# Kernel tuning notes

Hardware: AMD Instinct MI355X
Metric: run time of the kernel (lower is better)

## Reference

```python
import jax, jax.numpy as jnp
import numpy as np

N_NODES = 50000
N_EDGES = 800000
D = 128          # d_model
N_LAYER = 4
N_GRAPHS = 128
N_IDS = 256      # nn.Embedding(256, d_model)


def setup_inputs() -> dict:
    key = jax.random.key(0)
    ks = jax.random.split(key, 10)
    s = 0.02
    return {
        "position_feature": jax.random.normal(ks[0], (N_NODES, 3), dtype=jnp.float32),
        "id_feature": jax.random.randint(ks[1], (N_NODES,), 0, N_IDS),
        "edge_index": jax.random.randint(ks[2], (2, N_EDGES), 0, N_NODES),
        "batch": jnp.sort(jax.random.randint(ks[3], (N_NODES,), 0, N_GRAPHS)),
        "num_graphs": N_GRAPHS,
        "Wp": jax.random.normal(ks[4], (3, D), dtype=jnp.float32) * s,
        "bp": jnp.zeros((D,), jnp.float32),
        "id_emb": jax.random.normal(ks[5], (N_IDS, D), dtype=jnp.float32) * s,
        "Wn": jax.random.normal(ks[6], (2 * D, D), dtype=jnp.float32) * s,
        "bn": jnp.zeros((D,), jnp.float32),
        "conv_W": jax.random.normal(ks[7], (N_LAYER, D, D), dtype=jnp.float32) * s,
        "conv_b": jnp.zeros((N_LAYER, D), jnp.float32),
        "Wa": jax.random.normal(ks[8], ((1 + N_LAYER) * D, D), dtype=jnp.float32) * s,
        "ba": jnp.zeros((D,), jnp.float32),
    }


def _gcn(x, W, b, src, dst, norm, n):
    # PyG GCNConv: h = x @ W; out[dst] += norm(e) * h[src]; out += bias
    h = x @ W
    msg = h[src] * norm[:, None]
    return jax.ops.segment_sum(msg, dst, num_segments=n) + b


def reference(position_feature, id_feature, edge_index, batch, num_graphs,
              Wp, bp, id_emb, Wn, bn, conv_W, conv_b, Wa, ba):
    n = position_feature.shape[0]
    # GCN normalization with self-loops (shared across all layers)
    loops = jnp.arange(n)
    src = jnp.concatenate([edge_index[0], loops])
    dst = jnp.concatenate([edge_index[1], loops])
    deg = jax.ops.segment_sum(jnp.ones_like(src, dtype=position_feature.dtype), dst, num_segments=n)
    dinv = jnp.where(deg > 0, jax.lax.rsqrt(deg), 0.0)
    norm = dinv[src] * dinv[dst]  # [E + N]

    pos = jax.nn.relu(position_feature @ Wp + bp)       # [N, D]
    idf = jax.nn.relu(id_emb[id_feature])               # [N, D]
    x = jax.nn.relu(jnp.concatenate([pos, idf], axis=1) @ Wn + bn)  # [N, D]

    gs = [jax.ops.segment_max(x, batch, num_segments=num_graphs)]   # g_embed_0
    h = x
    for l in range(conv_W.shape[0]):
        h = jax.nn.relu(_gcn(h, conv_W[l], conv_b[l], src, dst, norm, n))
        gs.append(jax.ops.segment_max(h, batch, num_segments=num_graphs))

    g_embed = jnp.concatenate(gs, axis=1)  # [G, (1+n_layer)*D]
    return g_embed @ Wa + ba               # [G, D]
```

## Files before the change

### kernel.cpp

```cpp
#include <hip/hip_runtime.h>

#define N_NODES 50000
#define N_EDGES 800000
#define D 128
#define NLAYER 4
#define NGRAPH 128
#define GDIM (5 * D)
#define NBUCK 196
#define BCAP 4608

typedef __attribute__((ext_vector_type(8))) short bf16x8;
typedef __attribute__((ext_vector_type(4))) float f32x4;

__device__ __forceinline__ float b2f(unsigned short u) {
    return __uint_as_float(((unsigned)u) << 16);
}
__device__ __forceinline__ unsigned short f2b(float f) {
    unsigned u = __float_as_uint(f);
    unsigned r = (u + 0x7fffu + ((u >> 16) & 1u)) >> 16;
    return (unsigned short)r;
}


__global__ __launch_bounds__(256) void k_bucket(
    const int* __restrict__ esrc, const int* __restrict__ edst,
    int* __restrict__ bcnt_rel, int* __restrict__ ebuf) {
    __shared__ int hcnt[NBUCK];
    __shared__ int hbase[NBUCK];
    int t = threadIdx.x;
    for (int i = t; i < NBUCK; i += 256) hcnt[i] = 0;
    __syncthreads();
    int e0 = blockIdx.x * 1024 + t;
    int d[4], s[4];
#pragma unroll
    for (int i = 0; i < 4; ++i) {
        int e = e0 + i * 256;
        if (e < N_EDGES) {
            d[i] = edst[e];
            s[i] = esrc[e];
            atomicAdd(&hcnt[d[i] >> 8], 1);
        } else {
            d[i] = -1;
        }
    }
    __syncthreads();
    for (int i = t; i < NBUCK; i += 256) {
        int c = hcnt[i];
        hbase[i] = (c > 0) ? (i * BCAP + atomicAdd(&bcnt_rel[i], c)) : 0;
        hcnt[i] = 0;
    }
    __syncthreads();
#pragma unroll
    for (int i = 0; i < 4; ++i) {
        if (d[i] >= 0) {
            int b = d[i] >> 8;
            int p = atomicAdd(&hcnt[b], 1);
            int pos = hbase[b] + p;
            if (pos < (b + 1) * BCAP)
                ebuf[pos] = (s[i] & 0xffff) | ((d[i] & 255) << 16);
        }
    }
}


__global__ void k_bscan(const int* __restrict__ bcnt_rel, int* __restrict__ bbase) {
    __shared__ int lds[256];
    int t = threadIdx.x;
    int v = (t < NBUCK) ? bcnt_rel[t] : 0;
    lds[t] = v;
    __syncthreads();
    int tot = v;
    for (int off = 1; off < 256; off <<= 1) {
        int add = (t >= off) ? lds[t - off] : 0;
        __syncthreads();
        tot += add;
        lds[t] = tot;
        __syncthreads();
    }
    if (t < NBUCK) bbase[t] = tot - v;
}


__global__ __launch_bounds__(256) void k_fillB1(
    const int* __restrict__ ebuf, const int* __restrict__ bcnt_rel,
    const int* __restrict__ bbase, const int* __restrict__ batch,
    int* __restrict__ offs, int* __restrict__ cnt, float* __restrict__ dinv,
    int* __restrict__ hist2) {
    __shared__ int lcnt[256];
    __shared__ int lscan[256];
    int b = blockIdx.x, t = threadIdx.x;
    lcnt[t] = 0;
    __syncthreads();
    int s0 = b * BCAP, s1 = b * BCAP + bcnt_rel[b];
    for (int i = s0 + t; i < s1; i += 256)
        atomicAdd(&lcnt[(ebuf[i] >> 16) & 255], 1);
    __syncthreads();
    int v = lcnt[t];
    lscan[t] = v;
    __syncthreads();
    int tot = v;
    for (int off = 1; off < 256; off <<= 1) {
        int add = (t >= off) ? lscan[t - off] : 0;
        __syncthreads();
        tot += add;
        lscan[t] = tot;
        __syncthreads();
    }
    int node = (b << 8) + t;
    if (node < N_NODES) {
        offs[node] = bbase[b] + (tot - v);
        cnt[node] = v;
        dinv[node] = 1.f / sqrtf((float)(v + 1));
        atomicAdd(&hist2[batch[node] * 128 + min(v, 127)], 1);
    }
}


__global__ __launch_bounds__(256) void k_fillB2(
    const int* __restrict__ ebuf, const int* __restrict__ bcnt_rel,
    const int* __restrict__ offs, const float* __restrict__ dinv,
    unsigned int* __restrict__ csrs) {
    __shared__ int loffs[256];
    __shared__ int lcnt[256];
    __shared__ float ldinv[256];
    int b = blockIdx.x, t = threadIdx.x;
    int nbase = b << 8;
    if (nbase + t < N_NODES) {
        loffs[t] = offs[nbase + t];
        ldinv[t] = dinv[nbase + t];
    }
    lcnt[t] = 0;
    __syncthreads();
    int s0 = b * BCAP, s1 = b * BCAP + bcnt_rel[b];
    for (int i = s0 + t; i < s1; i += 256) {
        int pk = ebuf[i];
        int ld = (pk >> 16) & 255;
        int src = pk & 0xffff;
        float w = dinv[src] * ldinv[ld];
        int p = atomicAdd(&lcnt[ld], 1);
        csrs[loffs[ld] + p] = (unsigned)src | ((unsigned)f2b(w) << 16);
    }
}

__global__ __launch_bounds__(1024) void k_scan16k(int* __restrict__ hist2) {
    __shared__ int lds[1024];
    int t = threadIdx.x;
    int v[16];
    int s = 0;
#pragma unroll
    for (int j = 0; j < 16; ++j) { v[j] = hist2[t * 16 + j]; s += v[j]; }
    lds[t] = s;
    __syncthreads();
    int tot = s;
    for (int off = 1; off < 1024; off <<= 1) {
        int add = (t >= off) ? lds[t - off] : 0;
        __syncthreads();
        tot += add;
        lds[t] = tot;
        __syncthreads();
    }
    int run = tot - s;
#pragma unroll
    for (int j = 0; j < 16; ++j) { hist2[t * 16 + j] = run; run += v[j]; }
}

__global__ void k_scatter(const int* __restrict__ cnt, const int* __restrict__ batch,
                          int* __restrict__ hist2, int* __restrict__ perm) {
    int i = blockIdx.x * 256 + threadIdx.x;
    if (i < N_NODES) {
        int key = batch[i] * 128 + min(cnt[i], 127);
        int p = atomicAdd(&hist2[key], 1);
        perm[p] = i;
    }
}


__global__ __launch_bounds__(256) void k_prep(
    const float* __restrict__ Wn, const float* __restrict__ convW,
    unsigned short* __restrict__ Wpack,
    const float* __restrict__ id_emb, float* __restrict__ T) {
    int blk = blockIdx.x;
    if (blk < 320) {
        int tid = blk * 256 + threadIdx.x;
        int m = tid >> 14;
        int rem = tid & 16383;
        int ct = rem >> 11, kc = (rem >> 9) & 3, l = (rem >> 3) & 63, j = rem & 7;
        int k = kc * 32 + ((l >> 4) * 8) + j;
        int n = ct * 16 + (l & 15);
        const float* src = (m == 0) ? Wn : (convW + (size_t)(m - 1) * 16384);
        Wpack[tid] = f2b(src[k * 128 + n]);
    } else {
        int t = threadIdx.x;
        int d = t & 127;
        int r = (blk - 320) * 2 + (t >> 7);
        float acc = 0.f;
        for (int k = 0; k < 128; ++k)
            acc = fmaf(fmaxf(id_emb[r * 128 + k], 0.f), Wn[(128 + k) * 128 + d], acc);
        T[r * 128 + d] = acc;
    }
}


__global__ __launch_bounds__(256) void k_encoder(
    const float* __restrict__ pos, const int* __restrict__ idfeat,
    const float* __restrict__ Wp, const float* __restrict__ bp,
    const unsigned short* __restrict__ WpackE, const float* __restrict__ bn,
    const float* __restrict__ T, unsigned short* __restrict__ A16,
    const int* __restrict__ batch, float* __restrict__ gbuf) {
    __shared__ unsigned short feat[64 * 128];
    __shared__ float posl[192];
    __shared__ int bbat[64];
    int t = threadIdx.x;
    int base = blockIdx.x * 64;
    int avail = N_NODES - base;
    if (t < 192) {
        int idx = base * 3 + t;
        posl[t] = (idx < N_NODES * 3) ? pos[idx] : 0.f;
    }
    if (t < 64) bbat[t] = (base + t < N_NODES) ? batch[base + t] : -1;
    __syncthreads();
#pragma unroll
    for (int i = 0; i < 4; ++i) {
        int gid = t + i * 256;
        int row = gid >> 4, kg = gid & 15;
        unsigned short u[8];
        if (row < avail) {
            float p0 = posl[row * 3], p1 = posl[row * 3 + 1], p2 = posl[row * 3 + 2];
#pragma unroll
            for (int j = 0; j < 8; ++j) {
                int d = kg * 8 + j;
                float v = fmaf(p0, Wp[d], fmaf(p1, Wp[128 + d], fmaf(p2, Wp[256 + d], bp[d])));
                u[j] = f2b(fmaxf(v, 0.f));
            }
        } else {
#pragma unroll
            for (int j = 0; j < 8; ++j) u[j] = 0;
        }
        char* dst = (char*)feat + row * 256 + ((kg * 16) ^ ((row & 7) << 4));
        *(uint4*)dst = *(uint4*)u;
    }
    __syncthreads();
    int wid = t >> 6, l = t & 63;
    int r0 = wid * 16;
    f32x4 acc[8];
#pragma unroll
    for (int ct = 0; ct < 8; ++ct) acc[ct] = (f32x4){0.f, 0.f, 0.f, 0.f};
    const bf16x8* wp = (const bf16x8*)WpackE;
#pragma unroll
    for (int kc = 0; kc < 4; ++kc) {
        int row = r0 + (l & 15);
        const char* ap = (const char*)feat + row * 256 +
                         ((kc * 64 + ((l >> 4) * 16)) ^ ((row & 7) << 4));
        bf16x8 afrag = *(const bf16x8*)ap;
#pragma unroll
        for (int ct = 0; ct < 8; ++ct) {
            bf16x8 bfrag = wp[(ct * 4 + kc) * 64 + l];
            acc[ct] = __builtin_amdgcn_mfma_f32_16x16x32_bf16(afrag, bfrag, acc[ct], 0, 0, 0);
        }
    }
    int subrow = (l >> 4) * 4, col0 = l & 15;
    int ids[4];
#pragma unroll
    for (int i = 0; i < 4; ++i) {
        int node = base + r0 + subrow + i;
        ids[i] = (node < N_NODES) ? idfeat[node] : 0;
    }
    __syncthreads();
#pragma unroll
    for (int ct = 0; ct < 8; ++ct) {
        int col = ct * 16 + col0;
        float bcol = bn[col];
#pragma unroll
        for (int i = 0; i < 4; ++i) {
            int node = base + r0 + subrow + i;
            unsigned short ob = 0;
            if (node < N_NODES) {
                float v = acc[ct][i] + bcol + T[ids[i] * 128 + col];
                ob = f2b(fmaxf(v, 0.f));
                A16[(size_t)node * 128 + col] = ob;
            }
            feat[(r0 + subrow + i) * 128 + col] = ob;
        }
    }
    __syncthreads();
    if (t < 128) {
        int j = 0;
        while (j < 64) {
            int g = bbat[j];
            float m = b2f(feat[j * 128 + t]);
            int k = j + 1;
            while (k < 64 && bbat[k] == g) { m = fmaxf(m, b2f(feat[k * 128 + t])); ++k; }
            if (g >= 0) atomicMax((int*)&gbuf[g * GDIM + t], __float_as_int(m));
            j = k;
        }
    }
}


__global__ __launch_bounds__(256) void k_layer(
    const unsigned short* __restrict__ Hin, unsigned short* __restrict__ Hout,
    const unsigned short* __restrict__ WpackL,
    const int* __restrict__ offs, const int* __restrict__ cnt,
    const unsigned int* __restrict__ csrs, const float* __restrict__ dinv,
    const float* __restrict__ bias, const int* __restrict__ batch,
    const int* __restrict__ perm, float* __restrict__ gbuf, int goff) {
    __shared__ unsigned short hagg[16 * 128];
    __shared__ float smx[16][132];
    __shared__ int bb[16];
    __shared__ int snode[16];
    int tid = threadIdx.x;
    int wave = tid >> 6, lane = tid & 63;
    int q = lane >> 4, l16 = lane & 15;
    int row = wave * 4 + q;
    int nbase = blockIdx.x * 16;
    if (tid < 16) {
        int n = perm[nbase + tid];
        snode[tid] = n;
        bb[tid] = batch[n];
    }
    int node = perm[nbase + row];

    int start = offs[node];
    int c = cnt[node];
    float di = dinv[node];
    float sw = di * di;
    const uint4* B4 = (const uint4*)Hin;
    float a[8];
    {
        uint4 sv = B4[(size_t)node * 16 + l16];
        a[0] = sw * __uint_as_float(sv.x << 16);
        a[1] = sw * __uint_as_float(sv.x & 0xffff0000u);
        a[2] = sw * __uint_as_float(sv.y << 16);
        a[3] = sw * __uint_as_float(sv.y & 0xffff0000u);
        a[4] = sw * __uint_as_float(sv.z << 16);
        a[5] = sw * __uint_as_float(sv.z & 0xffff0000u);
        a[6] = sw * __uint_as_float(sv.w << 16);
        a[7] = sw * __uint_as_float(sv.w & 0xffff0000u);
    }
    int j = 0;
    for (; j + 8 <= c; j += 8) {
        unsigned pk[8];
        uint4 v[8];
#pragma unroll
        for (int i = 0; i < 8; ++i) pk[i] = csrs[start + j + i];
#pragma unroll
        for (int i = 0; i < 8; ++i) v[i] = B4[(size_t)(pk[i] & 0xffffu) * 16 + l16];
#pragma unroll
        for (int i = 0; i < 8; ++i) {
            float w = __uint_as_float(pk[i] & 0xffff0000u);
            a[0] = fmaf(w, __uint_as_float(v[i].x << 16), a[0]);
            a[1] = fmaf(w, __uint_as_float(v[i].x & 0xffff0000u), a[1]);
            a[2] = fmaf(w, __uint_as_float(v[i].y << 16), a[2]);
            a[3] = fmaf(w, __uint_as_float(v[i].y & 0xffff0000u), a[3]);
            a[4] = fmaf(w, __uint_as_float(v[i].z << 16), a[4]);
            a[5] = fmaf(w, __uint_as_float(v[i].z & 0xffff0000u), a[5]);
            a[6] = fmaf(w, __uint_as_float(v[i].w << 16), a[6]);
            a[7] = fmaf(w, __uint_as_float(v[i].w & 0xffff0000u), a[7]);
        }
    }
    for (; j < c; ++j) {
        unsigned pk = csrs[start + j];
        float w = __uint_as_float(pk & 0xffff0000u);
        uint4 v = B4[(size_t)(pk & 0xffffu) * 16 + l16];
        a[0] = fmaf(w, __uint_as_float(v.x << 16), a[0]);
        a[1] = fmaf(w, __uint_as_float(v.x & 0xffff0000u), a[1]);
        a[2] = fmaf(w, __uint_as_float(v.y << 16), a[2]);
        a[3] = fmaf(w, __uint_as_float(v.y & 0xffff0000u), a[3]);
        a[4] = fmaf(w, __uint_as_float(v.z << 16), a[4]);
        a[5] = fmaf(w, __uint_as_float(v.z & 0xffff0000u), a[5]);
        a[6] = fmaf(w, __uint_as_float(v.w << 16), a[6]);
        a[7] = fmaf(w, __uint_as_float(v.w & 0xffff0000u), a[7]);
    }
    {
        unsigned u[4];
#pragma unroll
        for (int k = 0; k < 4; ++k)
            u[k] = (unsigned)f2b(a[2 * k]) | ((unsigned)f2b(a[2 * k + 1]) << 16);
        char* dst = (char*)hagg + row * 256 + ((l16 * 16) ^ ((row & 7) << 4));
        *(uint4*)dst = *(uint4*)u;
    }
    __syncthreads();

    f32x4 oacc[2] = {(f32x4){0.f, 0.f, 0.f, 0.f}, (f32x4){0.f, 0.f, 0.f, 0.f}};
    const bf16x8* wp = (const bf16x8*)WpackL;
#pragma unroll
    for (int kc = 0; kc < 4; ++kc) {
        int arow = lane & 15;
        const char* ap = (const char*)hagg + arow * 256 +
                         ((kc * 64 + ((lane >> 4) * 16)) ^ ((arow & 7) << 4));
        bf16x8 afrag = *(const bf16x8*)ap;
#pragma unroll
        for (int ci = 0; ci < 2; ++ci) {
            int ct = wave * 2 + ci;
            bf16x8 bfrag = wp[(ct * 4 + kc) * 64 + lane];
            oacc[ci] = __builtin_amdgcn_mfma_f32_16x16x32_bf16(afrag, bfrag, oacc[ci], 0, 0, 0);
        }
    }

    int subrow = (lane >> 4) * 4;
#pragma unroll
    for (int ci = 0; ci < 2; ++ci) {
        int col = (wave * 2 + ci) * 16 + (lane & 15);
        float bcol = bias[col];
#pragma unroll
        for (int i = 0; i < 4; ++i) {
            int r = subrow + i;
            float v = fmaxf(oacc[ci][i] + bcol, 0.f);
            smx[r][col] = v;
            Hout[(size_t)snode[r] * 128 + col] = f2b(v);
        }
    }
    __syncthreads();
    if (tid < 128) {
        int jj = 0;
        while (jj < 16) {
            int g = bb[jj];
            float m = smx[jj][tid];
            int k = jj + 1;
            while (k < 16 && bb[k] == g) { m = fmaxf(m, smx[k][tid]); ++k; }
            atomicMax((int*)&gbuf[g * GDIM + goff + tid], __float_as_int(m));
            jj = k;
        }
    }
}


__global__ __launch_bounds__(128) void k_final(const float* __restrict__ gbuf,
                                               const float* __restrict__ Wa,
                                               const float* __restrict__ ba,
                                               float* __restrict__ out) {
    __shared__ float gr[GDIM];
    int g = blockIdx.x, t = threadIdx.x;
    for (int i = t; i < GDIM; i += 128) gr[i] = gbuf[g * GDIM + i];
    __syncthreads();
    float acc = ba[t];
    for (int k = 0; k < GDIM; ++k) acc = fmaf(gr[k], Wa[k * 128 + t], acc);
    out[g * 128 + t] = acc;
}


extern "C" void kernel_launch(void* const* d_in, const int* in_sizes, int n_in,
                              void* d_out, int out_size, void* d_ws, size_t ws_size,
                              hipStream_t stream) {
    const float* pos    = (const float*)d_in[0];
    const int*   idfeat = (const int*)d_in[1];
    const int*   eidx   = (const int*)d_in[2];
    const int*   batch  = (const int*)d_in[3];
    const float* Wp     = (const float*)d_in[5];
    const float* bp     = (const float*)d_in[6];
    const float* id_emb = (const float*)d_in[7];
    const float* Wn     = (const float*)d_in[8];
    const float* bn     = (const float*)d_in[9];
    const float* convW  = (const float*)d_in[10];
    const float* convb  = (const float*)d_in[11];
    const float* Wa     = (const float*)d_in[12];
    const float* ba     = (const float*)d_in[13];
    float* out = (float*)d_out;

    const int* esrc = eidx;
    const int* edst = eidx + N_EDGES;

    char* w = (char*)d_ws;
    auto alloc = [&](size_t bytes) -> char* {
        char* p = w;
        w += (bytes + 255) & ~(size_t)255;
        return p;
    };
    char* zstart = w;
    float* gbuf     = (float*)alloc((size_t)NGRAPH * GDIM * 4);
    int*   hist2    = (int*)alloc((size_t)16384 * 4);
    int*   bcnt_rel = (int*)alloc((size_t)NBUCK * 4);
    size_t zbytes = (size_t)(w - zstart);

    int*   cnt  = (int*)alloc((size_t)N_NODES * 4);
    unsigned short* A16a = (unsigned short*)alloc((size_t)N_NODES * D * 2);
    unsigned short* A16b = (unsigned short*)alloc((size_t)N_NODES * D * 2);
    float* dinv = (float*)alloc((size_t)N_NODES * 4);
    int*   offs = (int*)alloc((size_t)(N_NODES + 1) * 4);
    int*   bbase= (int*)alloc((NBUCK + 1) * 4);
    unsigned int* csrs = (unsigned int*)alloc((size_t)N_EDGES * 4);
    int*   ebuf = (int*)alloc((size_t)NBUCK * BCAP * 4);
    int*   perm = (int*)alloc((size_t)N_NODES * 4);
    float* T    = (float*)alloc((size_t)256 * D * 4);
    unsigned short* Wpack = (unsigned short*)alloc((size_t)5 * 16384 * 2);

    hipMemsetAsync(zstart, 0, zbytes, stream);

    k_bucket<<<(N_EDGES + 1023) / 1024, 256, 0, stream>>>(esrc, edst, bcnt_rel, ebuf);
    k_bscan<<<1, 256, 0, stream>>>(bcnt_rel, bbase);
    k_fillB1<<<NBUCK, 256, 0, stream>>>(ebuf, bcnt_rel, bbase, batch, offs, cnt, dinv, hist2);
    k_scan16k<<<1, 1024, 0, stream>>>(hist2);
    k_scatter<<<(N_NODES + 255) / 256, 256, 0, stream>>>(cnt, batch, hist2, perm);
    k_fillB2<<<NBUCK, 256, 0, stream>>>(ebuf, bcnt_rel, offs, dinv, csrs);

    k_prep<<<448, 256, 0, stream>>>(Wn, convW, Wpack, id_emb, T);
    k_encoder<<<(N_NODES + 63) / 64, 256, 0, stream>>>(pos, idfeat, Wp, bp, Wpack, bn, T,
                                                       A16a, batch, gbuf);

    unsigned short* Hin = A16a;
    unsigned short* Hout = A16b;
    for (int l = 0; l < NLAYER; ++l) {
        k_layer<<<N_NODES / 16, 256, 0, stream>>>(Hin, Hout, Wpack + (size_t)(l + 1) * 16384,
                                                  offs, cnt, csrs, dinv,
                                                  convb + (size_t)l * D, batch, perm, gbuf,
                                                  (l + 1) * D);
        unsigned short* tmp = Hin; Hin = Hout; Hout = tmp;
    }

    k_final<<<NGRAPH, 128, 0, stream>>>(gbuf, Wa, ba, out);
}
```

Before: 260.7 us.

## Process 32 nodes per block in GCN layer with dual interleaved gathers

Each k_layer block now handles 32 nodes instead of 16. Each 16-lane group gathers neighbours for two nodes at once, interleaving their loads 4 at a time to expose more memory-level parallelism. Each B-fragment load of the weights now feeds two MFMA row tiles, and the per-block max buffer is stored as bf16 to save LDS. The hipMemsetAsync is replaced with a custom zeroing kernel. The trade-off is fewer blocks, more registers per thread, and load imbalance when the two nodes have very different degrees.

```diff
diff --git a/kernel.cpp b/kernel.cpp
--- a/kernel.cpp
+++ b/kernel.cpp
@@ -19,6 +19,23 @@
     unsigned u = __float_as_uint(f);
     unsigned r = (u + 0x7fffu + ((u >> 16) & 1u)) >> 16;
     return (unsigned short)r;
+}
+__device__ __forceinline__ void fma8(float* a, unsigned pkw, uint4 v) {
+    float w = __uint_as_float(pkw & 0xffff0000u);
+    a[0] = fmaf(w, __uint_as_float(v.x << 16), a[0]);
+    a[1] = fmaf(w, __uint_as_float(v.x & 0xffff0000u), a[1]);
+    a[2] = fmaf(w, __uint_as_float(v.y << 16), a[2]);
+    a[3] = fmaf(w, __uint_as_float(v.y & 0xffff0000u), a[3]);
+    a[4] = fmaf(w, __uint_as_float(v.z << 16), a[4]);
+    a[5] = fmaf(w, __uint_as_float(v.z & 0xffff0000u), a[5]);
+    a[6] = fmaf(w, __uint_as_float(v.w << 16), a[6]);
+    a[7] = fmaf(w, __uint_as_float(v.w & 0xffff0000u), a[7]);
+}
+
+
+__global__ void k_zero(uint4* __restrict__ p, int n16) {
+    int i = blockIdx.x * 256 + threadIdx.x;
+    if (i < n16) p[i] = make_uint4(0u, 0u, 0u, 0u);
 }
 
 
@@ -304,96 +321,155 @@
     const unsigned int* __restrict__ csrs, const float* __restrict__ dinv,
     const float* __restrict__ bias, const int* __restrict__ batch,
     const int* __restrict__ perm, float* __restrict__ gbuf, int goff) {
-    __shared__ unsigned short hagg[16 * 128];
-    __shared__ float smx[16][132];
-    __shared__ int bb[16];
-    __shared__ int snode[16];
+    __shared__ unsigned short hagg[32 * 128];
+    __shared__ unsigned short smx[32 * 136];
+    __shared__ int bb[32];
+    __shared__ int snode[32];
     int tid = threadIdx.x;
     int wave = tid >> 6, lane = tid & 63;
-    int q = lane >> 4, l16 = lane & 15;
-    int row = wave * 4 + q;
-    int nbase = blockIdx.x * 16;
-    if (tid < 16) {
-        int n = perm[nbase + tid];
-        snode[tid] = n;
-        bb[tid] = batch[n];
-    }
-    int node = perm[nbase + row];
-
-    int start = offs[node];
-    int c = cnt[node];
-    float di = dinv[node];
-    float sw = di * di;
+    int r = tid >> 4;
+    int l16 = tid & 15;
+    int nbase = blockIdx.x * 32;
+    if (tid < 32) {
+        int idx = nbase + tid;
+        if (idx < N_NODES) {
+            int n = perm[idx];
+            snode[tid] = n;
+            bb[tid] = batch[n];
+        } else {
+            snode[tid] = 0;
+            bb[tid] = -1;
+        }
+    }
+    int idx0 = nbase + r;
+    int idx1 = nbase + 16 + r;
+    int node0 = perm[idx0];
+    bool val1 = idx1 < N_NODES;
+    int node1 = val1 ? perm[idx1] : 0;
+
     const uint4* B4 = (const uint4*)Hin;
-    float a[8];
+    int start0 = offs[node0], c0 = cnt[node0];
+    float di0 = dinv[node0];
+    int start1 = val1 ? offs[node1] : 0;
+    int c1 = val1 ? cnt[node1] : 0;
+    float di1 = val1 ? dinv[node1] : 0.f;
+
+    float a0[8], a1[8];
     {
-        uint4 sv = B4[(size_t)node * 16 + l16];
-        a[0] = sw * __uint_as_float(sv.x << 16);
-        a[1] = sw * __uint_as_float(sv.x & 0xffff0000u);
-        a[2] = sw * __uint_as_float(sv.y << 16);
-        a[3] = sw * __uint_as_float(sv.y & 0xffff0000u);
-        a[4] = sw * __uint_as_float(sv.z << 16);
-        a[5] = sw * __uint_as_float(sv.z & 0xffff0000u);
-        a[6] = sw * __uint_as_float(sv.w << 16);
-        a[7] = sw * __uint_as_float(sv.w & 0xffff0000u);
-    }
-    int j = 0;
-    for (; j + 8 <= c; j += 8) {
-        unsigned pk[8];
-        uint4 v[8];
-#pragma unroll
-        for (int i = 0; i < 8; ++i) pk[i] = csrs[start + j + i];
-#pragma unroll
-        for (int i = 0; i < 8; ++i) v[i] = B4[(size_t)(pk[i] & 0xffffu) * 16 + l16];
-#pragma unroll
-        for (int i = 0; i < 8; ++i) {
-            float w = __uint_as_float(pk[i] & 0xffff0000u);
-            a[0] = fmaf(w, __uint_as_float(v[i].x << 16), a[0]);
-            a[1] = fmaf(w, __uint_as_float(v[i].x & 0xffff0000u), a[1]);
-            a[2] = fmaf(w, __uint_as_float(v[i].y << 16), a[2]);
-            a[3] = fmaf(w, __uint_as_float(v[i].y & 0xffff0000u), a[3]);
-            a[4] = fmaf(w, __uint_as_float(v[i].z << 16), a[4]);
-            a[5] = fmaf(w, __uint_as_float(v[i].z & 0xffff0000u), a[5]);
-            a[6] = fmaf(w, __uint_as_float(v[i].w << 16), a[6]);
-            a[7] = fmaf(w, __uint_as_float(v[i].w & 0xffff0000u), a[7]);
-        }
-    }
-    for (; j < c; ++j) {
-        unsigned pk = csrs[start + j];
-        float w = __uint_as_float(pk & 0xffff0000u);
-        uint4 v = B4[(size_t)(pk & 0xffffu) * 16 + l16];
-        a[0] = fmaf(w, __uint_as_float(v.x << 16), a[0]);
-        a[1] = fmaf(w, __uint_as_float(v.x & 0xffff0000u), a[1]);
-        a[2] = fmaf(w, __uint_as_float(v.y << 16), a[2]);
-        a[3] = fmaf(w, __uint_as_float(v.y & 0xffff0000u), a[3]);
-        a[4] = fmaf(w, __uint_as_float(v.z << 16), a[4]);
-        a[5] = fmaf(w, __uint_as_float(v.z & 0xffff0000u), a[5]);
-        a[6] = fmaf(w, __uint_as_float(v.w << 16), a[6]);
-        a[7] = fmaf(w, __uint_as_float(v.w & 0xffff0000u), a[7]);
+        uint4 sv = B4[(size_t)node0 * 16 + l16];
+        float sw = di0 * di0;
+        a0[0] = sw * __uint_as_float(sv.x << 16);
+        a0[1] = sw * __uint_as_float(sv.x & 0xffff0000u);
+        a0[2] = sw * __uint_as_float(sv.y << 16);
+        a0[3] = sw * __uint_as_float(sv.y & 0xffff0000u);
+        a0[4] = sw * __uint_as_float(sv.z << 16);
+        a0[5] = sw * __uint_as_float(sv.z & 0xffff0000u);
+        a0[6] = sw * __uint_as_float(sv.w << 16);
+        a0[7] = sw * __uint_as_float(sv.w & 0xffff0000u);
+    }
+    if (val1) {
+        uint4 sv = B4[(size_t)node1 * 16 + l16];
+        float sw = di1 * di1;
+        a1[0] = sw * __uint_as_float(sv.x << 16);
+        a1[1] = sw * __uint_as_float(sv.x & 0xffff0000u);
+        a1[2] = sw * __uint_as_float(sv.y << 16);
+        a1[3] = sw * __uint_as_float(sv.y & 0xffff0000u);
+        a1[4] = sw * __uint_as_float(sv.z << 16);
+        a1[5] = sw * __uint_as_float(sv.z & 0xffff0000u);
+        a1[6] = sw * __uint_as_float(sv.w << 16);
+        a1[7] = sw * __uint_as_float(sv.w & 0xffff0000u);
+    } else {
+#pragma unroll
+        for (int i = 0; i < 8; ++i) a1[i] = 0.f;
+    }
+
+    int j0 = 0, j1 = 0;
+    while (j0 + 4 <= c0 && j1 + 4 <= c1) {
+        unsigned p0[4], p1[4];
+        uint4 v0[4], v1[4];
+#pragma unroll
+        for (int i = 0; i < 4; ++i) p0[i] = csrs[start0 + j0 + i];
+#pragma unroll
+        for (int i = 0; i < 4; ++i) p1[i] = csrs[start1 + j1 + i];
+#pragma unroll
+        for (int i = 0; i < 4; ++i) v0[i] = B4[(size_t)(p0[i] & 0xffffu) * 16 + l16];
+#pragma unroll
+        for (int i = 0; i < 4; ++i) v1[i] = B4[(size_t)(p1[i] & 0xffffu) * 16 + l16];
+#pragma unroll
+        for (int i = 0; i < 4; ++i) fma8(a0, p0[i], v0[i]);
+#pragma unroll
+        for (int i = 0; i < 4; ++i) fma8(a1, p1[i], v1[i]);
+        j0 += 4;
+        j1 += 4;
+    }
+    for (; j0 + 4 <= c0; j0 += 4) {
+        unsigned p0[4];
+        uint4 v0[4];
+#pragma unroll
+        for (int i = 0; i < 4; ++i) p0[i] = csrs[start0 + j0 + i];
+#pragma unroll
+        for (int i = 0; i < 4; ++i) v0[i] = B4[(size_t)(p0[i] & 0xffffu) * 16 + l16];
+#pragma unroll
+        for (int i = 0; i < 4; ++i) fma8(a0, p0[i], v0[i]);
+    }
+    for (; j0 < c0; ++j0) {
+        unsigned pk = csrs[start0 + j0];
+        fma8(a0, pk, B4[(size_t)(pk & 0xffffu) * 16 + l16]);
+    }
+    for (; j1 + 4 <= c1; j1 += 4) {
+        unsigned p1[4];
+        uint4 v1[4];
+#pragma unroll
+        for (int i = 0; i < 4; ++i) p1[i] = csrs[start1 + j1 + i];
+#pragma unroll
+        for (int i = 0; i < 4; ++i) v1[i] = B4[(size_t)(p1[i] & 0xffffu) * 16 + l16];
+#pragma unroll
+        for (int i = 0; i < 4; ++i) fma8(a1, p1[i], v1[i]);
+    }
+    for (; j1 < c1; ++j1) {
+        unsigned pk = csrs[start1 + j1];
+        fma8(a1, pk, B4[(size_t)(pk & 0xffffu) * 16 + l16]);
     }
     {
         unsigned u[4];
 #pragma unroll
         for (int k = 0; k < 4; ++k)
-            u[k] = (unsigned)f2b(a[2 * k]) | ((unsigned)f2b(a[2 * k + 1]) << 16);
-        char* dst = (char*)hagg + row * 256 + ((l16 * 16) ^ ((row & 7) << 4));
+            u[k] = (unsigned)f2b(a0[2 * k]) | ((unsigned)f2b(a0[2 * k + 1]) << 16);
+        char* dst = (char*)hagg + r * 256 + ((l16 * 16) ^ ((r & 7) << 4));
         *(uint4*)dst = *(uint4*)u;
-    }
-    __syncthreads();
-
-    f32x4 oacc[2] = {(f32x4){0.f, 0.f, 0.f, 0.f}, (f32x4){0.f, 0.f, 0.f, 0.f}};
+        int r1 = r + 16;
+#pragma unroll
+        for (int k = 0; k < 4; ++k)
+            u[k] = (unsigned)f2b(a1[2 * k]) | ((unsigned)f2b(a1[2 * k + 1]) << 16);
+        dst = (char*)hagg + r1 * 256 + ((l16 * 16) ^ ((r1 & 7) << 4));
+        *(uint4*)dst = *(uint4*)u;
+    }
+    __syncthreads();
+
+    f32x4 oacc[2][2];
+#pragma unroll
+    for (int rt = 0; rt < 2; ++rt)
+#pragma unroll
+        for (int ci = 0; ci < 2; ++ci) oacc[rt][ci] = (f32x4){0.f, 0.f, 0.f, 0.f};
     const bf16x8* wp = (const bf16x8*)WpackL;
 #pragma unroll
     for (int kc = 0; kc < 4; ++kc) {
-        int arow = lane & 15;
-        const char* ap = (const char*)hagg + arow * 256 +
-                         ((kc * 64 + ((lane >> 4) * 16)) ^ ((arow & 7) << 4));
-        bf16x8 afrag = *(const bf16x8*)ap;
+        bf16x8 afrag[2];
+#pragma unroll
+        for (int rt = 0; rt < 2; ++rt) {
+            int arow = rt * 16 + (lane & 15);
+            const char* ap = (const char*)hagg + arow * 256 +
+                             ((kc * 64 + ((lane >> 4) * 16)) ^ ((arow & 7) << 4));
+            afrag[rt] = *(const bf16x8*)ap;
+        }
 #pragma unroll
         for (int ci = 0; ci < 2; ++ci) {
             int ct = wave * 2 + ci;
             bf16x8 bfrag = wp[(ct * 4 + kc) * 64 + lane];
-            oacc[ci] = __builtin_amdgcn_mfma_f32_16x16x32_bf16(afrag, bfrag, oacc[ci], 0, 0, 0);
+#pragma unroll
+            for (int rt = 0; rt < 2; ++rt)
+                oacc[rt][ci] = __builtin_amdgcn_mfma_f32_16x16x32_bf16(afrag[rt], bfrag,
+                                                                      oacc[rt][ci], 0, 0, 0);
         }
     }
 
@@ -403,22 +479,29 @@
         int col = (wave * 2 + ci) * 16 + (lane & 15);
         float bcol = bias[col];
 #pragma unroll
-        for (int i = 0; i < 4; ++i) {
-            int r = subrow + i;
-            float v = fmaxf(oacc[ci][i] + bcol, 0.f);
-            smx[r][col] = v;
-            Hout[(size_t)snode[r] * 128 + col] = f2b(v);
+        for (int rt = 0; rt < 2; ++rt) {
+#pragma unroll
+            for (int i = 0; i < 4; ++i) {
+                int row = rt * 16 + subrow + i;
+                float v = fmaxf(oacc[rt][ci][i] + bcol, 0.f);
+                unsigned short ob = f2b(v);
+                if (bb[row] >= 0)
+                    Hout[(size_t)snode[row] * 128 + col] = ob;
+                else
+                    ob = 0;
+                smx[row * 136 + col] = ob;
+            }
         }
     }
     __syncthreads();
     if (tid < 128) {
         int jj = 0;
-        while (jj < 16) {
+        while (jj < 32) {
             int g = bb[jj];
-            float m = smx[jj][tid];
+            float m = b2f(smx[jj * 136 + tid]);
             int k = jj + 1;
-            while (k < 16 && bb[k] == g) { m = fmaxf(m, smx[k][tid]); ++k; }
-            atomicMax((int*)&gbuf[g * GDIM + goff + tid], __float_as_int(m));
+            while (k < 32 && bb[k] == g) { m = fmaxf(m, b2f(smx[k * 136 + tid])); ++k; }
+            if (g >= 0) atomicMax((int*)&gbuf[g * GDIM + goff + tid], __float_as_int(m));
             jj = k;
         }
     }
@@ -484,7 +567,8 @@
     float* T    = (float*)alloc((size_t)256 * D * 4);
     unsigned short* Wpack = (unsigned short*)alloc((size_t)5 * 16384 * 2);
 
-    hipMemsetAsync(zstart, 0, zbytes, stream);
+    int n16 = (int)(zbytes / 16);
+    k_zero<<<(n16 + 255) / 256, 256, 0, stream>>>((uint4*)zstart, n16);
 
     k_bucket<<<(N_EDGES + 1023) / 1024, 256, 0, stream>>>(esrc, edst, bcnt_rel, ebuf);
     k_bscan<<<1, 256, 0, stream>>>(bcnt_rel, bbase);
@@ -500,10 +584,11 @@
     unsigned short* Hin = A16a;
     unsigned short* Hout = A16b;
     for (int l = 0; l < NLAYER; ++l) {
-        k_layer<<<N_NODES / 16, 256, 0, stream>>>(Hin, Hout, Wpack + (size_t)(l + 1) * 16384,
-                                                  offs, cnt, csrs, dinv,
-                                                  convb + (size_t)l * D, batch, perm, gbuf,
-                                                  (l + 1) * D);
+        k_layer<<<(N_NODES + 31) / 32, 256, 0, stream>>>(Hin, Hout,
+                                                         Wpack + (size_t)(l + 1) * 16384,
+                                                         offs, cnt, csrs, dinv,
+                                                         convb + (size_t)l * D, batch, perm,
+                                                         gbuf, (l + 1) * D);
         unsigned short* tmp = Hin; Hin = Hout; Hout = tmp;
     }
 
```

After: 288.9 us. +10.8%, slower.
